# Optimization experiments

Measured on AMD Instinct MI355X. Metric: run time of the kernel, lower is better.

Reference implementation:

```python
import jax, jax.numpy as jnp
import numpy as np


def _make_area_table():
    # Surrogate for create_table_neighbour_code_to_surface_area((1,1,1)):
    # a fixed 256-entry lookup that is exactly 0 for the all-empty (0) and
    # all-full (255) neighbour codes and strictly positive otherwise, which
    # preserves the structure the loss relies on (gt_surface = area > 0,
    # gt_foreground = code==255, gt_background = code==0).
    pop = np.array([bin(c).count("1") for c in range(256)], dtype=np.float32)
    return (0.5 * np.minimum(pop, 8.0 - pop)).astype(np.float32)


def _conv3d(x, w):
    # x: [B,1,D,H,W], w: [1,1,2,2,2], VALID 2x2x2 sliding window
    return jax.lax.conv_general_dilated(
        x, w, window_strides=(1, 1, 1), padding="VALID",
        dimension_numbers=("NCDHW", "OIDHW", "NCDHW"))


def setup_inputs() -> dict:
    key = jax.random.key(0)
    k1, k2 = jax.random.split(key)
    B, D, H, W = 2, 128, 256, 256
    preds = jax.random.normal(k1, (B, 1, D, H, W), dtype=jnp.float32)
    targets = jax.random.randint(k2, (B, 1, D, H, W), 0, 2).astype(jnp.float32)
    power = (2.0 ** jnp.arange(8, dtype=jnp.float32)).reshape(1, 1, 2, 2, 2)
    kernel = jnp.ones((1, 1, 2, 2, 2), dtype=jnp.float32)
    area = jnp.asarray(_make_area_table())
    return {"preds": preds, "targets": targets, "power": power,
            "kernel": kernel, "area": area}


def reference(preds, targets, power, kernel, area):
    eps = 1e-5
    bsz = preds.shape[0]

    # log-prob that all 8 voxels of each 2x2x2 cube are foreground / background
    fg = jnp.exp(_conv3d(jax.nn.log_sigmoid(preds), kernel)).reshape(bsz, -1)
    bg = jnp.exp(_conv3d(jax.nn.log_sigmoid(-preds), kernel)).reshape(bsz, -1)
    surf = 1.0 - fg - bg

    # neighbour codes from binary targets (no grad path)
    codes = jax.lax.stop_gradient(_conv3d(targets, power)).astype(jnp.int32).reshape(bsz, -1)
    gt_area = area[codes.reshape(-1)].reshape(bsz, -1)
    gt_fg = (codes == 255).astype(jnp.float32)
    gt_bg = (codes == 0).astype(jnp.float32)
    gt_surf = (gt_area > 0).astype(jnp.float32)

    fg_dice = (2.0 * jnp.sum(fg * gt_fg, -1) + eps) / (jnp.sum(fg, -1) + jnp.sum(gt_fg, -1) + eps)
    bg_dice = (2.0 * jnp.sum(bg * gt_bg, -1) + eps) / (jnp.sum(bg, -1) + jnp.sum(gt_bg, -1) + eps)
    surf_dice = (2.0 * jnp.sum(surf * gt_area, -1) + eps) / (jnp.sum((surf + gt_surf) * gt_area, -1) + eps)

    dice = (fg_dice + bg_dice + surf_dice) / 3.0
    return 1.0 - jnp.mean(dice)
```

## Files before the change

kernel.cpp:

```cpp
#include <hip/hip_runtime.h>

typedef float f2 __attribute__((ext_vector_type(2)));

#define DD 128
#define HH 256
#define WW 256
#define OD 127
#define SLICE_F (HH*WW)
#define CHUNK 16
#define TEN_B 9216
#define SLOT_B 18432
#define NBUF 4
#define AS1 __attribute__((address_space(1)))
#define AS3 __attribute__((address_space(3)))

#define WAITP() do { if (wv < 2) asm volatile("s_waitcnt vmcnt(10)" ::: "memory"); \
                     else        asm volatile("s_waitcnt vmcnt(8)"  ::: "memory"); } while (0)
#define WAIT1() do { if (wv < 2) asm volatile("s_waitcnt vmcnt(5)"  ::: "memory"); \
                     else        asm volatile("s_waitcnt vmcnt(4)"  ::: "memory"); } while (0)
#define WAIT0() asm volatile("s_waitcnt vmcnt(0)" ::: "memory")

struct Sl { f2 uu2[4]; f2 vv2[4]; f2 ps[4]; };

__device__ __forceinline__ void stage_slice(const float* __restrict__ pB,
                                            const float* __restrict__ tB,
                                            int s, char* lb, int h0, int wv, int lane)
{
    #pragma unroll
    for (int i = 0; i < 5; ++i) {
        const int L = i * 4 + wv;
        if (L < 18) {
            const int T = (L >= 9) ? 1 : 0;
            const int r = L - T * 9;
            const int grow = min(h0 + r, HH - 1);
            const float* g = (T ? tB : pB)
                           + ((size_t)s << 16) + ((size_t)grow << 8) + (lane << 2);
            void* l = lb + T * TEN_B + r * 1024 + lane * 16;
            __builtin_amdgcn_global_load_lds((const AS1 void*)g, (AS3 void*)l, 16, 0, 0);
        }
    }
}

__device__ __forceinline__ void make_sl(const char* lb, int wv, int lane, Sl& S)
{
    const float* sp = (const float*)lb;
    const float* st = (const float*)(lb + TEN_B);
    const int ro = ((wv << 1) << 8) + (lane << 2);
    const float4 p0 = *(const float4*)(sp + ro);
    const float4 p1 = *(const float4*)(sp + ro + 256);
    const float4 p2 = *(const float4*)(sp + ro + 512);
    const float4 t0 = *(const float4*)(st + ro);
    const float4 t1 = *(const float4*)(st + ro + 256);
    const float4 t2 = *(const float4*)(st + ro + 512);

    float u0x=__expf(p0.x), u0y=__expf(p0.y), u0z=__expf(p0.z), u0w=__expf(p0.w);
    float u1x=__expf(p1.x), u1y=__expf(p1.y), u1z=__expf(p1.z), u1w=__expf(p1.w);
    float u2x=__expf(p2.x), u2y=__expf(p2.y), u2z=__expf(p2.z), u2w=__expf(p2.w);

    f2 uA0 = {u0x,u1x}, uB0 = {u1x,u2x};
    f2 uA1 = {u0y,u1y}, uB1 = {u1y,u2y};
    f2 uA2 = {u0z,u1z}, uB2 = {u1z,u2z};
    f2 uA3 = {u0w,u1w}, uB3 = {u1w,u2w};

    f2 W0 = uA0*uB0, W1 = uA1*uB1, W2 = uA2*uB2, W3 = uA3*uB3;
    f2 Q0 = (uA0+1.f)*(uB0+1.f);
    f2 Q1 = (uA1+1.f)*(uB1+1.f);
    f2 Q2 = (uA2+1.f)*(uB2+1.f);
    f2 Q3 = (uA3+1.f)*(uB3+1.f);
    f2 W4, Q4;
    W4.x = __shfl_down(W0.x, 1); W4.y = __shfl_down(W0.y, 1);
    Q4.x = __shfl_down(Q0.x, 1); Q4.y = __shfl_down(Q0.y, 1);

    S.uu2[0]=W0*W1; S.uu2[1]=W1*W2; S.uu2[2]=W2*W3; S.uu2[3]=W3*W4;
    S.vv2[0]=Q0*Q1; S.vv2[1]=Q1*Q2; S.vv2[2]=Q2*Q3; S.vv2[3]=Q3*Q4;

    f2 cs0 = {t0.x+t1.x, t1.x+t2.x};
    f2 cs1 = {t0.y+t1.y, t1.y+t2.y};
    f2 cs2 = {t0.z+t1.z, t1.z+t2.z};
    f2 cs3 = {t0.w+t1.w, t1.w+t2.w};
    f2 cs4; cs4.x = __shfl_down(cs0.x, 1); cs4.y = __shfl_down(cs0.y, 1);
    S.ps[0]=cs0+cs1; S.ps[1]=cs1+cs2; S.ps[2]=cs2+cs3; S.ps[3]=cs3+cs4;
}

__device__ __forceinline__ void do_cubes(const Sl& P, const Sl& C,
        const f2 vAll, const f2 v3,
        f2& aFG, f2& aF255, f2& aBG, f2& aBG0, f2& aSFA,
        f2& c255, f2& c0, f2& cMN)
{
    #pragma unroll
    for (int j = 0; j < 4; ++j) {
        f2 E = P.uu2[j] * C.uu2[j];
        f2 Q = P.vv2[j] * C.vv2[j];
        f2 vj = (j == 3) ? v3 : vAll;
        f2 r; r.x = __builtin_amdgcn_rcpf(Q.x); r.y = __builtin_amdgcn_rcpf(Q.y);
        r *= vj;
        f2 fg = E * r;
        f2 pop = P.ps[j] + C.ps[j];
        f2 i255, i0, mn;
        i255.x = fmaxf(pop.x - 7.f, 0.f); i255.y = fmaxf(pop.y - 7.f, 0.f);
        i0.x   = fmaxf(1.f - pop.x, 0.f); i0.y   = fmaxf(1.f - pop.y, 0.f);
        mn.x   = 4.f - fabsf(pop.x - 4.f); mn.y = 4.f - fabsf(pop.y - 4.f);
        mn *= vj;
        aFG  += fg;
        aBG  += r;
        aF255 = fg * i255 + aF255;
        aBG0  = r  * i0   + aBG0;
        c255  = i255 * vj + c255;
        c0    = i0   * vj + c0;
        aSFA  = (fg + r) * mn + aSFA;
        cMN  += mn;
    }
}

#define LAYER(SRC, DST)                                                        \
    do {                                                                       \
        if (t + 3 <= NT) {                                                     \
            stage_slice(pB, tB, d0 + t + 3, smem + sw * SLOT_B, h0, wv, lane); \
            WAITP();         \
        } else if (t + 2 <= NT) {                                              \
            WAIT1();                                 \
        } else {                                                               \
            WAIT0();                                                           \
        }                                                                      \
        __builtin_amdgcn_s_barrier();                                          \
        __builtin_amdgcn_sched_barrier(0);                                     \
        make_sl(smem + sr * SLOT_B, wv, lane, DST);                            \
        do_cubes(SRC, DST, vAll, v3, aFG, aF255, aBG, aBG0, aSFA, c255, c0, cMN); \
        sr = (sr + 1) & 3;                                                     \
        sw = (sw + 1) & 3;                                                     \
    } while (0)

__global__ __launch_bounds__(256, 2)
void loss_main(const float* __restrict__ preds,
               const float* __restrict__ targets,
               float* __restrict__ ws)
{
    __shared__ __align__(16) char smem[NBUF * SLOT_B];
    __shared__ float red[32];

    const int lane = threadIdx.x & 63;
    const int wv   = threadIdx.x >> 6;

    const int nid = ((blockIdx.x & 7) << 6) + (blockIdx.x >> 3);
    const int x = nid & 31;
    const int y = (nid >> 5) & 7;
    const int b = nid >> 8;

    const int h0 = x << 3;
    const int d0 = y << 4;
    const int NT = min(CHUNK, OD - d0);

    const float* pB = preds   + (size_t)b * DD * SLICE_F;
    const float* tB = targets + (size_t)b * DD * SLICE_F;

    const int   myrow = h0 + (wv << 1);
    const float rv1 = (myrow + 1 < HH - 1) ? 1.f : 0.f;
    const float v63 = (lane == 63) ? 0.f : 1.f;
    const f2 vAll = {1.f, rv1};
    const f2 v3   = {v63, v63 * rv1};

    f2 aFG={0,0}, aF255={0,0}, aBG={0,0}, aBG0={0,0}, aSFA={0,0};
    f2 c255={0,0}, c0={0,0}, cMN={0,0};

    stage_slice(pB, tB, d0,     smem,             h0, wv, lane);
    stage_slice(pB, tB, d0 + 1, smem + SLOT_B,    h0, wv, lane);
    stage_slice(pB, tB, d0 + 2, smem + 2*SLOT_B,  h0, wv, lane);
    WAITP();
    __builtin_amdgcn_s_barrier();
    __builtin_amdgcn_sched_barrier(0);

    Sl A, B;
    make_sl(smem, wv, lane, A);

    int sr = 1, sw = 3;
    int t = 0;
    for (;;) {
        LAYER(A, B);
        if (++t >= NT) break;
        LAYER(B, A);
        if (++t >= NT) break;
    }

    float acc[8] = {aFG.x+aFG.y, aF255.x+aF255.y, c255.x+c255.y,
                    aBG.x+aBG.y, aBG0.x+aBG0.y,   c0.x+c0.y,
                    aSFA.x+aSFA.y, cMN.x+cMN.y};
    #pragma unroll
    for (int i = 0; i < 8; ++i) {
        float v = acc[i];
        #pragma unroll
        for (int off = 32; off > 0; off >>= 1) v += __shfl_xor(v, off);
        acc[i] = v;
    }
    float mine = acc[0];
    mine = (lane == 1) ? acc[1] : mine;
    mine = (lane == 2) ? acc[2] : mine;
    mine = (lane == 3) ? acc[3] : mine;
    mine = (lane == 4) ? acc[4] : mine;
    mine = (lane == 5) ? acc[5] : mine;
    mine = (lane == 6) ? acc[6] : mine;
    mine = (lane == 7) ? acc[7] : mine;
    if (lane < 8) red[wv * 8 + lane] = mine;
    __syncthreads();
    if (wv == 0 && lane < 8)
        ws[nid * 8 + lane] = red[lane] + red[8 + lane] + red[16 + lane] + red[24 + lane];
}

__global__ void loss_final(const float* __restrict__ ws, float* __restrict__ out)
{
    __shared__ float part[16][17];
    __shared__ float S[16];
    const int tid = threadIdx.x;
    const int c = tid >> 4, sub = tid & 15;
    const int bb = c >> 3, s = c & 7;
    float v = 0.f;
    #pragma unroll 4
    for (int k = 0; k < 16; ++k) {
        int nid = bb * 256 + sub * 16 + k;
        v += ws[nid * 8 + s];
    }
    part[c][sub] = v;
    __syncthreads();
    if (tid < 16) {
        float q = 0.f;
        #pragma unroll
        for (int i = 0; i < 16; ++i) q += part[tid][i];
        S[tid] = q;
    }
    __syncthreads();
    if (tid == 0) {
        const float eps = 1e-5f;
        float dice = 0.f;
        #pragma unroll
        for (int b2 = 0; b2 < 2; ++b2) {
            const float* q = S + b2 * 8;
            float fg_dice = (2.f*q[1] + eps) / (q[0] + q[2] + eps);
            float bg_dice = (2.f*q[4] + eps) / (q[3] + q[5] + eps);
            float q6 = 0.5f * q[6];
            float q7 = 0.5f * q[7];
            float ss = q7 - q6;
            float sf_dice = (2.f*ss + eps) / (ss + q7 + eps);
            dice += fg_dice + bg_dice + sf_dice;
        }
        out[0] = 1.f - dice * (1.f/6.f);
    }
}

extern "C" void kernel_launch(void* const* d_in, const int* in_sizes, int n_in,
                              void* d_out, int out_size, void* d_ws, size_t ws_size,
                              hipStream_t stream)
{
    const float* preds   = (const float*)d_in[0];
    const float* targets = (const float*)d_in[1];
    float* ws = (float*)d_ws;

    loss_main<<<512, 256, 0, stream>>>(preds, targets, ws);
    loss_final<<<1, 256, 0, stream>>>(ws, (float*)d_out);
}
```

Before: 32.63 us.

## Pre-pack binary targets into bitmasks and halve depth chunk for more blocks

```diff
diff --git a/kernel.cpp b/kernel.cpp
--- a/kernel.cpp
+++ b/kernel.cpp
@@ -7,51 +7,76 @@
 #define WW 256
 #define OD 127
 #define SLICE_F (HH*WW)
-#define CHUNK 16
-#define TEN_B 9216
-#define SLOT_B 18432
+#define CHUNK 8
+#define PRED_B 9216
+#define BITS_B 512
+#define SLOT_B (PRED_B + BITS_B)
 #define NBUF 4
+#define WS_BITS_OFF 32768
 #define AS1 __attribute__((address_space(1)))
 #define AS3 __attribute__((address_space(3)))
 
-#define WAITP() do { if (wv < 2) asm volatile("s_waitcnt vmcnt(10)" ::: "memory"); \
-                     else        asm volatile("s_waitcnt vmcnt(8)"  ::: "memory"); } while (0)
-#define WAIT1() do { if (wv < 2) asm volatile("s_waitcnt vmcnt(5)"  ::: "memory"); \
-                     else        asm volatile("s_waitcnt vmcnt(4)"  ::: "memory"); } while (0)
+#define WAITP() do { if (wv < 3) asm volatile("s_waitcnt vmcnt(6)" ::: "memory"); \
+                     else        asm volatile("s_waitcnt vmcnt(4)" ::: "memory"); } while (0)
+#define WAIT1() do { if (wv < 3) asm volatile("s_waitcnt vmcnt(3)" ::: "memory"); \
+                     else        asm volatile("s_waitcnt vmcnt(2)" ::: "memory"); } while (0)
 #define WAIT0() asm volatile("s_waitcnt vmcnt(0)" ::: "memory")
 
 struct Sl { f2 uu2[4]; f2 vv2[4]; f2 ps[4]; };
 
+__global__ __launch_bounds__(256)
+void pack_bits(const float* __restrict__ t, unsigned int* __restrict__ bits)
+{
+    const int tid = blockIdx.x * 256 + threadIdx.x;
+    const float4* p = (const float4*)(t + ((size_t)tid << 5));
+    unsigned int acc = 0;
+    #pragma unroll
+    for (int i = 0; i < 8; ++i) {
+        float4 v = p[i];
+        unsigned int n = ((__float_as_uint(v.x) >> 29) & 1u)
+                       | (((__float_as_uint(v.y) >> 29) & 1u) << 1)
+                       | (((__float_as_uint(v.z) >> 29) & 1u) << 2)
+                       | (((__float_as_uint(v.w) >> 29) & 1u) << 3);
+        acc |= n << (i * 4);
+    }
+    bits[tid] = acc;
+}
+
+__device__ __forceinline__ void pred_row(const float* __restrict__ pB, int s,
+                                         int h0, int r, char* lb, int lane)
+{
+    const int grow = min(h0 + r, HH - 1);
+    const float* g = pB + ((size_t)s << 16) + ((size_t)grow << 8) + (lane << 2);
+    __builtin_amdgcn_global_load_lds((const AS1 void*)g,
+        (AS3 void*)(lb + r * 1024 + lane * 16), 16, 0, 0);
+}
+
+__device__ __forceinline__ void bits_half(const unsigned int* __restrict__ bB, int s,
+                                          int h0, int half, char* lb, int lane)
+{
+    const int grow = min(h0 + (half << 3) + (lane >> 3), HH - 1);
+    const unsigned int* g = bB + (((size_t)s * HH + grow) << 3) + (lane & 7);
+    __builtin_amdgcn_global_load_lds((const AS1 void*)g,
+        (AS3 void*)(lb + PRED_B + half * 256 + lane * 4), 4, 0, 0);
+}
+
 __device__ __forceinline__ void stage_slice(const float* __restrict__ pB,
-                                            const float* __restrict__ tB,
+                                            const unsigned int* __restrict__ bB,
                                             int s, char* lb, int h0, int wv, int lane)
 {
-    #pragma unroll
-    for (int i = 0; i < 5; ++i) {
-        const int L = i * 4 + wv;
-        if (L < 18) {
-            const int T = (L >= 9) ? 1 : 0;
-            const int r = L - T * 9;
-            const int grow = min(h0 + r, HH - 1);
-            const float* g = (T ? tB : pB)
-                           + ((size_t)s << 16) + ((size_t)grow << 8) + (lane << 2);
-            void* l = lb + T * TEN_B + r * 1024 + lane * 16;
-            __builtin_amdgcn_global_load_lds((const AS1 void*)g, (AS3 void*)l, 16, 0, 0);
-        }
-    }
+    if (wv == 0)      { pred_row(pB,s,h0,0,lb,lane); pred_row(pB,s,h0,4,lb,lane); pred_row(pB,s,h0,8,lb,lane); }
+    else if (wv == 1) { pred_row(pB,s,h0,1,lb,lane); pred_row(pB,s,h0,5,lb,lane); bits_half(bB,s,h0,0,lb,lane); }
+    else if (wv == 2) { pred_row(pB,s,h0,2,lb,lane); pred_row(pB,s,h0,6,lb,lane); bits_half(bB,s,h0,1,lb,lane); }
+    else              { pred_row(pB,s,h0,3,lb,lane); pred_row(pB,s,h0,7,lb,lane); }
 }
 
 __device__ __forceinline__ void make_sl(const char* lb, int wv, int lane, Sl& S)
 {
     const float* sp = (const float*)lb;
-    const float* st = (const float*)(lb + TEN_B);
     const int ro = ((wv << 1) << 8) + (lane << 2);
     const float4 p0 = *(const float4*)(sp + ro);
     const float4 p1 = *(const float4*)(sp + ro + 256);
     const float4 p2 = *(const float4*)(sp + ro + 512);
-    const float4 t0 = *(const float4*)(st + ro);
-    const float4 t1 = *(const float4*)(st + ro + 256);
-    const float4 t2 = *(const float4*)(st + ro + 512);
 
     float u0x=__expf(p0.x), u0y=__expf(p0.y), u0z=__expf(p0.z), u0w=__expf(p0.w);
     float u1x=__expf(p1.x), u1y=__expf(p1.y), u1z=__expf(p1.z), u1w=__expf(p1.w);
@@ -74,12 +99,23 @@
     S.uu2[0]=W0*W1; S.uu2[1]=W1*W2; S.uu2[2]=W2*W3; S.uu2[3]=W3*W4;
     S.vv2[0]=Q0*Q1; S.vv2[1]=Q1*Q2; S.vv2[2]=Q2*Q3; S.vv2[3]=Q3*Q4;
 
-    f2 cs0 = {t0.x+t1.x, t1.x+t2.x};
-    f2 cs1 = {t0.y+t1.y, t1.y+t2.y};
-    f2 cs2 = {t0.z+t1.z, t1.z+t2.z};
-    f2 cs3 = {t0.w+t1.w, t1.w+t2.w};
-    f2 cs4; cs4.x = __shfl_down(cs0.x, 1); cs4.y = __shfl_down(cs0.y, 1);
-    S.ps[0]=cs0+cs1; S.ps[1]=cs1+cs2; S.ps[2]=cs2+cs3; S.ps[3]=cs3+cs4;
+    const unsigned int* bl = (const unsigned int*)(lb + PRED_B);
+    const int r = wv << 1;
+    const int q = lane >> 3;
+    const int sh = (lane & 7) << 2;
+    unsigned int a0 = bl[r*8 + q],     a1 = bl[r*8 + q + 1];
+    unsigned int b0 = bl[(r+1)*8 + q], b1 = bl[(r+1)*8 + q + 1];
+    unsigned int c0 = bl[(r+2)*8 + q], c1 = bl[(r+2)*8 + q + 1];
+    unsigned int m0 = (unsigned int)(((((unsigned long long)a1) << 32) | a0) >> sh) & 0x1Fu;
+    unsigned int m1 = (unsigned int)(((((unsigned long long)b1) << 32) | b0) >> sh) & 0x1Fu;
+    unsigned int m2 = (unsigned int)(((((unsigned long long)c1) << 32) | c0) >> sh) & 0x1Fu;
+    unsigned int M01 = m0 | (m1 << 8);
+    unsigned int M12 = m1 | (m2 << 8);
+    #pragma unroll
+    for (int j = 0; j < 4; ++j) {
+        S.ps[j].x = (float)__popc((M01 >> j) & 0x303u);
+        S.ps[j].y = (float)__popc((M12 >> j) & 0x303u);
+    }
 }
 
 __device__ __forceinline__ void do_cubes(const Sl& P, const Sl& C,
@@ -115,10 +151,10 @@
 #define LAYER(SRC, DST)                                                        \
     do {                                                                       \
         if (t + 3 <= NT) {                                                     \
-            stage_slice(pB, tB, d0 + t + 3, smem + sw * SLOT_B, h0, wv, lane); \
+            stage_slice(pB, bB, d0 + t + 3, smem + sw * SLOT_B, h0, wv, lane); \
             WAITP();         \
         } else if (t + 2 <= NT) {                                              \
-            WAIT1();                                 \
+            WAIT1();                                                           \
         } else {                                                               \
             WAIT0();                                                           \
         }                                                                      \
@@ -130,9 +166,9 @@
         sw = (sw + 1) & 3;                                                     \
     } while (0)
 
-__global__ __launch_bounds__(256, 2)
+__global__ __launch_bounds__(256, 4)
 void loss_main(const float* __restrict__ preds,
-               const float* __restrict__ targets,
+               const unsigned int* __restrict__ bits,
                float* __restrict__ ws)
 {
     __shared__ __align__(16) char smem[NBUF * SLOT_B];
@@ -141,17 +177,17 @@
     const int lane = threadIdx.x & 63;
     const int wv   = threadIdx.x >> 6;
 
-    const int nid = ((blockIdx.x & 7) << 6) + (blockIdx.x >> 3);
+    const int nid = ((blockIdx.x & 7) << 7) + (blockIdx.x >> 3);
     const int x = nid & 31;
-    const int y = (nid >> 5) & 7;
-    const int b = nid >> 8;
+    const int y = (nid >> 5) & 15;
+    const int b = nid >> 9;
 
     const int h0 = x << 3;
-    const int d0 = y << 4;
+    const int d0 = y << 3;
     const int NT = min(CHUNK, OD - d0);
 
-    const float* pB = preds   + (size_t)b * DD * SLICE_F;
-    const float* tB = targets + (size_t)b * DD * SLICE_F;
+    const float*        pB = preds + (size_t)b * DD * SLICE_F;
+    const unsigned int* bB = bits  + (size_t)b * DD * HH * 8;
 
     const int   myrow = h0 + (wv << 1);
     const float rv1 = (myrow + 1 < HH - 1) ? 1.f : 0.f;
@@ -162,9 +198,9 @@
     f2 aFG={0,0}, aF255={0,0}, aBG={0,0}, aBG0={0,0}, aSFA={0,0};
     f2 c255={0,0}, c0={0,0}, cMN={0,0};
 
-    stage_slice(pB, tB, d0,     smem,             h0, wv, lane);
-    stage_slice(pB, tB, d0 + 1, smem + SLOT_B,    h0, wv, lane);
-    stage_slice(pB, tB, d0 + 2, smem + 2*SLOT_B,  h0, wv, lane);
+    stage_slice(pB, bB, d0,     smem,            h0, wv, lane);
+    stage_slice(pB, bB, d0 + 1, smem + SLOT_B,   h0, wv, lane);
+    stage_slice(pB, bB, d0 + 2, smem + 2*SLOT_B, h0, wv, lane);
     WAITP();
     __builtin_amdgcn_s_barrier();
     __builtin_amdgcn_sched_barrier(0);
@@ -214,8 +250,8 @@
     const int bb = c >> 3, s = c & 7;
     float v = 0.f;
     #pragma unroll 4
-    for (int k = 0; k < 16; ++k) {
-        int nid = bb * 256 + sub * 16 + k;
+    for (int k = 0; k < 32; ++k) {
+        int nid = bb * 512 + sub * 32 + k;
         v += ws[nid * 8 + s];
     }
     part[c][sub] = v;
@@ -252,7 +288,9 @@
     const float* preds   = (const float*)d_in[0];
     const float* targets = (const float*)d_in[1];
     float* ws = (float*)d_ws;
-
-    loss_main<<<512, 256, 0, stream>>>(preds, targets, ws);
+    unsigned int* bitsbuf = (unsigned int*)((char*)d_ws + WS_BITS_OFF);
+
+    pack_bits<<<2048, 256, 0, stream>>>(targets, bitsbuf);
+    loss_main<<<1024, 256, 0, stream>>>(preds, bitsbuf, ws);
     loss_final<<<1, 256, 0, stream>>>(ws, (float*)d_out);
 }
```

Result: slower. 44.82 us (+37.4%).

## Fuse final reduction into main kernel via atomic ticket; balance staging loads per wave

Applied to the files above, without the earlier changes.

```diff
diff --git a/kernel.cpp b/kernel.cpp
--- a/kernel.cpp
+++ b/kernel.cpp
@@ -11,13 +11,12 @@
 #define TEN_B 9216
 #define SLOT_B 18432
 #define NBUF 4
+#define NBLK 512
 #define AS1 __attribute__((address_space(1)))
 #define AS3 __attribute__((address_space(3)))
 
-#define WAITP() do { if (wv < 2) asm volatile("s_waitcnt vmcnt(10)" ::: "memory"); \
-                     else        asm volatile("s_waitcnt vmcnt(8)"  ::: "memory"); } while (0)
-#define WAIT1() do { if (wv < 2) asm volatile("s_waitcnt vmcnt(5)"  ::: "memory"); \
-                     else        asm volatile("s_waitcnt vmcnt(4)"  ::: "memory"); } while (0)
+#define WAITP() asm volatile("s_waitcnt vmcnt(9)" ::: "memory")
+#define WAIT1() asm volatile("s_waitcnt vmcnt(4)" ::: "memory")
 #define WAIT0() asm volatile("s_waitcnt vmcnt(0)" ::: "memory")
 
 struct Sl { f2 uu2[4]; f2 vv2[4]; f2 ps[4]; };
@@ -26,9 +25,10 @@
                                             const float* __restrict__ tB,
                                             int s, char* lb, int h0, int wv, int lane)
 {
+    const int w2 = (s & 1) ? (3 - wv) : wv;
     #pragma unroll
     for (int i = 0; i < 5; ++i) {
-        const int L = i * 4 + wv;
+        const int L = i * 4 + w2;
         if (L < 18) {
             const int T = (L >= 9) ? 1 : 0;
             const int r = L - T * 9;
@@ -116,9 +116,9 @@
     do {                                                                       \
         if (t + 3 <= NT) {                                                     \
             stage_slice(pB, tB, d0 + t + 3, smem + sw * SLOT_B, h0, wv, lane); \
-            WAITP();         \
+            WAITP();              \
         } else if (t + 2 <= NT) {                                              \
-            WAIT1();                                 \
+            WAIT1();                                                           \
         } else {                                                               \
             WAIT0();                                                           \
         }                                                                      \
@@ -133,10 +133,13 @@
 __global__ __launch_bounds__(256, 2)
 void loss_main(const float* __restrict__ preds,
                const float* __restrict__ targets,
-               float* __restrict__ ws)
+               float* __restrict__ ws,
+               float* __restrict__ out)
 {
     __shared__ __align__(16) char smem[NBUF * SLOT_B];
     __shared__ float red[32];
+    __shared__ float fin[256];
+    __shared__ unsigned int ticket;
 
     const int lane = threadIdx.x & 63;
     const int wv   = threadIdx.x >> 6;
@@ -203,45 +206,46 @@
     __syncthreads();
     if (wv == 0 && lane < 8)
         ws[nid * 8 + lane] = red[lane] + red[8 + lane] + red[16 + lane] + red[24 + lane];
-}
-
-__global__ void loss_final(const float* __restrict__ ws, float* __restrict__ out)
-{
-    __shared__ float part[16][17];
-    __shared__ float S[16];
-    const int tid = threadIdx.x;
-    const int c = tid >> 4, sub = tid & 15;
-    const int bb = c >> 3, s = c & 7;
-    float v = 0.f;
-    #pragma unroll 4
-    for (int k = 0; k < 16; ++k) {
-        int nid = bb * 256 + sub * 16 + k;
-        v += ws[nid * 8 + s];
-    }
-    part[c][sub] = v;
+
+    __threadfence();
     __syncthreads();
-    if (tid < 16) {
-        float q = 0.f;
+    if (threadIdx.x == 0)
+        ticket = atomicAdd((unsigned int*)(ws + NBLK * 8), 1u);
+    __syncthreads();
+    if ((ticket & (NBLK - 1u)) == NBLK - 1u) {
+        __threadfence();
+        const int tid = threadIdx.x;
+        const int s = tid & 7, k = tid >> 3;
+        float v = 0.f;
         #pragma unroll
-        for (int i = 0; i < 16; ++i) q += part[tid][i];
-        S[tid] = q;
-    }
-    __syncthreads();
-    if (tid == 0) {
-        const float eps = 1e-5f;
-        float dice = 0.f;
-        #pragma unroll
-        for (int b2 = 0; b2 < 2; ++b2) {
-            const float* q = S + b2 * 8;
-            float fg_dice = (2.f*q[1] + eps) / (q[0] + q[2] + eps);
-            float bg_dice = (2.f*q[4] + eps) / (q[3] + q[5] + eps);
-            float q6 = 0.5f * q[6];
-            float q7 = 0.5f * q[7];
-            float ss = q7 - q6;
-            float sf_dice = (2.f*ss + eps) / (ss + q7 + eps);
-            dice += fg_dice + bg_dice + sf_dice;
+        for (int j = 0; j < 16; ++j)
+            v += ws[(k * 16 + j) * 8 + s];
+        fin[tid] = v;
+        __syncthreads();
+        if (tid < 16) {
+            const int b2 = tid >> 3, s2 = tid & 7;
+            float q = 0.f;
+            #pragma unroll
+            for (int k2 = 0; k2 < 16; ++k2) q += fin[(b2 * 16 + k2) * 8 + s2];
+            red[tid] = q;
         }
-        out[0] = 1.f - dice * (1.f/6.f);
+        __syncthreads();
+        if (tid == 0) {
+            const float eps = 1e-5f;
+            float dice = 0.f;
+            #pragma unroll
+            for (int b2 = 0; b2 < 2; ++b2) {
+                const float* q = red + b2 * 8;
+                float fg_dice = (2.f*q[1] + eps) / (q[0] + q[2] + eps);
+                float bg_dice = (2.f*q[4] + eps) / (q[3] + q[5] + eps);
+                float q6 = 0.5f * q[6];
+                float q7 = 0.5f * q[7];
+                float ss = q7 - q6;
+                float sf_dice = (2.f*ss + eps) / (ss + q7 + eps);
+                dice += fg_dice + bg_dice + sf_dice;
+            }
+            out[0] = 1.f - dice * (1.f/6.f);
+        }
     }
 }
 
@@ -253,6 +257,5 @@
     const float* targets = (const float*)d_in[1];
     float* ws = (float*)d_ws;
 
-    loss_main<<<512, 256, 0, stream>>>(preds, targets, ws);
-    loss_final<<<1, 256, 0, stream>>>(ws, (float*)d_out);
-}
+    loss_main<<<NBLK, 256, 0, stream>>>(preds, targets, ws, (float*)d_out);
+}
```

Result: slower. 69.21 us (+112.1%).

## Shrink LDS ring to three slots and raise occupancy with finer depth chunks

Applied to the files above, without the earlier changes.

```diff
diff --git a/kernel.cpp b/kernel.cpp
--- a/kernel.cpp
+++ b/kernel.cpp
@@ -7,18 +7,18 @@
 #define WW 256
 #define OD 127
 #define SLICE_F (HH*WW)
-#define CHUNK 16
-#define TEN_B 9216
-#define SLOT_B 18432
-#define NBUF 4
+#define CH 11
+#define PRED_B 8192
+#define TARG_B 9216
+#define SLOT_B 17408
+#define NBUF 3
+#define NBLK 768
 #define AS1 __attribute__((address_space(1)))
 #define AS3 __attribute__((address_space(3)))
 
-#define WAITP() do { if (wv < 2) asm volatile("s_waitcnt vmcnt(10)" ::: "memory"); \
-                     else        asm volatile("s_waitcnt vmcnt(8)"  ::: "memory"); } while (0)
-#define WAIT1() do { if (wv < 2) asm volatile("s_waitcnt vmcnt(5)"  ::: "memory"); \
-                     else        asm volatile("s_waitcnt vmcnt(4)"  ::: "memory"); } while (0)
+#define WAIT5() asm volatile("s_waitcnt vmcnt(5)" ::: "memory")
 #define WAIT0() asm volatile("s_waitcnt vmcnt(0)" ::: "memory")
+#define SB0()   __builtin_amdgcn_sched_barrier(0)
 
 struct Sl { f2 uu2[4]; f2 vv2[4]; f2 ps[4]; };
 
@@ -26,29 +26,43 @@
                                             const float* __restrict__ tB,
                                             int s, char* lb, int h0, int wv, int lane)
 {
+    const size_t so = ((size_t)s << 16);
     #pragma unroll
-    for (int i = 0; i < 5; ++i) {
+    for (int i = 0; i < 4; ++i) {
         const int L = i * 4 + wv;
-        if (L < 18) {
-            const int T = (L >= 9) ? 1 : 0;
-            const int r = L - T * 9;
-            const int grow = min(h0 + r, HH - 1);
-            const float* g = (T ? tB : pB)
-                           + ((size_t)s << 16) + ((size_t)grow << 8) + (lane << 2);
-            void* l = lb + T * TEN_B + r * 1024 + lane * 16;
-            __builtin_amdgcn_global_load_lds((const AS1 void*)g, (AS3 void*)l, 16, 0, 0);
-        }
-    }
-}
-
-__device__ __forceinline__ void make_sl(const char* lb, int wv, int lane, Sl& S)
+        const int T = (L >= 8) ? 1 : 0;
+        const int r = L & 7;
+        const int grow = min(h0 + r, HH - 1);
+        const float* g = (T ? tB : pB) + so + ((size_t)grow << 8) + (lane << 2);
+        void* l = lb + T * PRED_B + r * 1024 + lane * 16;
+        __builtin_amdgcn_global_load_lds((const AS1 void*)g, (AS3 void*)l, 16, 0, 0);
+    }
+    {
+        const int grow = min(h0 + 8, HH - 1);
+        const float* g = tB + so + ((size_t)grow << 8) + (wv << 6) + lane;
+        void* l = lb + PRED_B + 8 * 1024 + (wv << 8) + (lane << 2);
+        __builtin_amdgcn_global_load_lds((const AS1 void*)g, (AS3 void*)l, 4, 0, 0);
+    }
+}
+
+__device__ __forceinline__ float4 ld_p8(const float* __restrict__ pB, int s,
+                                        int h0, int lane)
+{
+    return *(const float4*)(pB + ((size_t)s << 16)
+                               + ((size_t)min(h0 + 8, HH - 1) << 8) + (lane << 2));
+}
+
+__device__ __forceinline__ void make_sl(const char* lb, int wv, int lane,
+                                        float4 p8, Sl& S)
 {
     const float* sp = (const float*)lb;
-    const float* st = (const float*)(lb + TEN_B);
+    const float* st = (const float*)(lb + PRED_B);
     const int ro = ((wv << 1) << 8) + (lane << 2);
     const float4 p0 = *(const float4*)(sp + ro);
     const float4 p1 = *(const float4*)(sp + ro + 256);
-    const float4 p2 = *(const float4*)(sp + ro + 512);
+    float4 p2;
+    if (wv < 3) p2 = *(const float4*)(sp + ro + 512);
+    else        p2 = p8;
     const float4 t0 = *(const float4*)(st + ro);
     const float4 t1 = *(const float4*)(st + ro + 256);
     const float4 t2 = *(const float4*)(st + ro + 512);
@@ -112,25 +126,22 @@
     }
 }
 
-#define LAYER(SRC, DST)                                                        \
+#define LAYER(SRC, DST, Pcons, Piss)                                           \
     do {                                                                       \
-        if (t + 3 <= NT) {                                                     \
+        if (t + 2 <= NT) WAIT5(); else WAIT0();                                \
+        __builtin_amdgcn_s_barrier();                                          \
+        if (wv == 3 && t + 2 <= NT) Piss = ld_p8(pB, d0 + t + 2, h0, lane);    \
+        SB0();                                                                 \
+        if (t + 3 <= NT)                                                       \
             stage_slice(pB, tB, d0 + t + 3, smem + sw * SLOT_B, h0, wv, lane); \
-            WAITP();         \
-        } else if (t + 2 <= NT) {                                              \
-            WAIT1();                                 \
-        } else {                                                               \
-            WAIT0();                                                           \
-        }                                                                      \
-        __builtin_amdgcn_s_barrier();                                          \
-        __builtin_amdgcn_sched_barrier(0);                                     \
-        make_sl(smem + sr * SLOT_B, wv, lane, DST);                            \
+        SB0();                                                                 \
+        make_sl(smem + sr * SLOT_B, wv, lane, Pcons, DST);                     \
         do_cubes(SRC, DST, vAll, v3, aFG, aF255, aBG, aBG0, aSFA, c255, c0, cMN); \
-        sr = (sr + 1) & 3;                                                     \
-        sw = (sw + 1) & 3;                                                     \
+        sr = (sr + 1 == NBUF) ? 0 : sr + 1;                                    \
+        sw = (sw + 1 == NBUF) ? 0 : sw + 1;                                    \
     } while (0)
 
-__global__ __launch_bounds__(256, 2)
+__global__ __launch_bounds__(256, 3)
 void loss_main(const float* __restrict__ preds,
                const float* __restrict__ targets,
                float* __restrict__ ws)
@@ -141,14 +152,15 @@
     const int lane = threadIdx.x & 63;
     const int wv   = threadIdx.x >> 6;
 
-    const int nid = ((blockIdx.x & 7) << 6) + (blockIdx.x >> 3);
-    const int x = nid & 31;
-    const int y = (nid >> 5) & 7;
-    const int b = nid >> 8;
+    const int nid  = (blockIdx.x & 7) * 96 + (blockIdx.x >> 3);
+    const int x    = nid & 31;
+    const int rest = nid >> 5;
+    const int y    = rest % 12;
+    const int b    = rest / 12;
 
     const int h0 = x << 3;
-    const int d0 = y << 4;
-    const int NT = min(CHUNK, OD - d0);
+    const int d0 = y * CH;
+    const int NT = min(CH, OD - d0);
 
     const float* pB = preds   + (size_t)b * DD * SLICE_F;
     const float* tB = targets + (size_t)b * DD * SLICE_F;
@@ -162,22 +174,30 @@
     f2 aFG={0,0}, aF255={0,0}, aBG={0,0}, aBG0={0,0}, aSFA={0,0};
     f2 c255={0,0}, c0={0,0}, cMN={0,0};
 
-    stage_slice(pB, tB, d0,     smem,             h0, wv, lane);
-    stage_slice(pB, tB, d0 + 1, smem + SLOT_B,    h0, wv, lane);
-    stage_slice(pB, tB, d0 + 2, smem + 2*SLOT_B,  h0, wv, lane);
-    WAITP();
+    float4 pA = {0,0,0,0}, pBv = pA;
+
+    if (wv == 3) pA = ld_p8(pB, d0, h0, lane);
+    SB0();
+    stage_slice(pB, tB, d0,     smem,            h0, wv, lane);
+    SB0();
+    if (wv == 3) pBv = ld_p8(pB, d0 + 1, h0, lane);
+    SB0();
+    stage_slice(pB, tB, d0 + 1, smem + SLOT_B,   h0, wv, lane);
+    SB0();
+    stage_slice(pB, tB, d0 + 2, smem + 2*SLOT_B, h0, wv, lane);
+    WAIT5();
     __builtin_amdgcn_s_barrier();
-    __builtin_amdgcn_sched_barrier(0);
+    SB0();
 
     Sl A, B;
-    make_sl(smem, wv, lane, A);
-
-    int sr = 1, sw = 3;
+    make_sl(smem, wv, lane, pA, A);
+
+    int sr = 1, sw = 0;
     int t = 0;
     for (;;) {
-        LAYER(A, B);
+        LAYER(A, B, pBv, pA);
         if (++t >= NT) break;
-        LAYER(B, A);
+        LAYER(B, A, pA, pBv);
         if (++t >= NT) break;
     }
 
@@ -207,23 +227,24 @@
 
 __global__ void loss_final(const float* __restrict__ ws, float* __restrict__ out)
 {
-    __shared__ float part[16][17];
+    __shared__ float fin[256];
     __shared__ float S[16];
     const int tid = threadIdx.x;
-    const int c = tid >> 4, sub = tid & 15;
-    const int bb = c >> 3, s = c & 7;
+    const int s = tid & 7, k = tid >> 3;
+    const int b2 = k >> 4;
     float v = 0.f;
     #pragma unroll 4
-    for (int k = 0; k < 16; ++k) {
-        int nid = bb * 256 + sub * 16 + k;
+    for (int j = 0; j < 24; ++j) {
+        int nid = b2 * 384 + (k & 15) * 24 + j;
         v += ws[nid * 8 + s];
     }
-    part[c][sub] = v;
+    fin[tid] = v;
     __syncthreads();
     if (tid < 16) {
+        const int bb = tid >> 3, s2 = tid & 7;
         float q = 0.f;
         #pragma unroll
-        for (int i = 0; i < 16; ++i) q += part[tid][i];
+        for (int k2 = 0; k2 < 16; ++k2) q += fin[((bb << 4) + k2) * 8 + s2];
         S[tid] = q;
     }
     __syncthreads();
@@ -231,8 +252,8 @@
         const float eps = 1e-5f;
         float dice = 0.f;
         #pragma unroll
-        for (int b2 = 0; b2 < 2; ++b2) {
-            const float* q = S + b2 * 8;
+        for (int bb = 0; bb < 2; ++bb) {
+            const float* q = S + bb * 8;
             float fg_dice = (2.f*q[1] + eps) / (q[0] + q[2] + eps);
             float bg_dice = (2.f*q[4] + eps) / (q[3] + q[5] + eps);
             float q6 = 0.5f * q[6];
@@ -253,6 +274,6 @@
     const float* targets = (const float*)d_in[1];
     float* ws = (float*)d_ws;
 
-    loss_main<<<512, 256, 0, stream>>>(preds, targets, ws);
+    loss_main<<<NBLK, 256, 0, stream>>>(preds, targets, ws);
     loss_final<<<1, 256, 0, stream>>>(ws, (float*)d_out);
 }
```

After: 35.70 us. +9.4%, slower.
